# Kernel tuning notes

Measured on AMD Instinct MI355X. Metric: run time of the kernel, lower is better.

## Reference

```python
import math
import jax, jax.numpy as jnp
import numpy as np

EMBED_DIM = 768
NUM_HEADS = 12
HEAD_DIM = EMBED_DIM // NUM_HEADS
NUM_BUCKETS = 32
MAX_DISTANCE = 128
B, S = 8, 1024


def setup_inputs() -> dict:
    key = jax.random.key(0)
    ks = jax.random.split(key, 16)
    sc = 0.02
    d = {
        "query": jax.random.normal(ks[0], (B, S, EMBED_DIM), jnp.float32),
        "Wq": jax.random.normal(ks[1], (EMBED_DIM, EMBED_DIM), jnp.float32) * sc,
        "bq": jnp.zeros((EMBED_DIM,), jnp.float32),
        "Wk": jax.random.normal(ks[2], (EMBED_DIM, EMBED_DIM), jnp.float32) * sc,
        "bk": jnp.zeros((EMBED_DIM,), jnp.float32),
        "Wv": jax.random.normal(ks[3], (EMBED_DIM, EMBED_DIM), jnp.float32) * sc,
        "bv": jnp.zeros((EMBED_DIM,), jnp.float32),
        "Wo": jax.random.normal(ks[4], (EMBED_DIM, EMBED_DIM), jnp.float32) * sc,
        "bo": jnp.zeros((EMBED_DIM,), jnp.float32),
        "rel_embed": jax.random.normal(ks[5], (NUM_BUCKETS, NUM_HEADS), jnp.float32) * sc,
        "gru_W": jax.random.normal(ks[6], (HEAD_DIM, 8), jnp.float32) * sc,
        "gru_b": jnp.zeros((8,), jnp.float32),
        "gru_const": jnp.ones((1, NUM_HEADS, 1, 1), jnp.float32),
    }
    return d


def _rel_pos_bias(rel_embed, seq_len):
    # bidirectional T5-style bucketing, matching WavLM._relative_positions_bucket
    ctx = jnp.arange(seq_len)[:, None]
    mem = jnp.arange(seq_len)[None, :]
    rp = mem - ctx  # [S, S]
    nb = NUM_BUCKETS // 2
    buckets = (rp > 0).astype(jnp.int32) * nb
    arp = jnp.abs(rp)
    max_exact = nb // 2
    is_small = arp < max_exact
    # truncation toward zero == astype for positive values; clamp to avoid log(0)
    large = max_exact + (
        jnp.log(jnp.maximum(arp, 1).astype(jnp.float32) / max_exact)
        / math.log(MAX_DISTANCE / max_exact)
        * (nb - max_exact)
    ).astype(jnp.int32)
    large = jnp.minimum(large, nb - 1)
    buckets = buckets + jnp.where(is_small, arp, large)
    # embedding lookup -> [S, S, H] -> [H, S, S]
    return rel_embed[buckets].transpose(2, 0, 1)


def reference(query, Wq, bq, Wk, bk, Wv, bv, Wo, bo, rel_embed, gru_W, gru_b, gru_const):
    b, s, e = query.shape
    h, d = NUM_HEADS, HEAD_DIM
    pos_bias = _rel_pos_bias(rel_embed, s)  # [H, S, S]

    # GRU-style gate computed from raw query, per head
    ql = query.reshape(b, s, h, d).transpose(0, 2, 1, 3)  # [B, H, S, D]
    g = jax.nn.sigmoid((ql @ gru_W + gru_b).reshape(b, h, s, 2, 4).sum(-1))  # [B,H,S,2]
    gate_a = g[..., 0:1]
    gate_b = g[..., 1:2]
    gate = gate_a * (gate_b * gru_const - 1.0) + 2.0  # [B, H, S, 1]
    attn_mask = gate * pos_bias[None]  # [B, H, S, S]

    scale = d ** (-0.5)
    q = (query @ Wq + bq).reshape(b, s, h, d).transpose(0, 2, 1, 3) * scale
    k = (query @ Wk + bk).reshape(b, s, h, d).transpose(0, 2, 1, 3)
    v = (query @ Wv + bv).reshape(b, s, h, d).transpose(0, 2, 1, 3)

    scores = jnp.einsum("bhqd,bhkd->bhqk", q, k) + attn_mask
    w = jax.nn.softmax(scores, axis=-1)  # max-subtraction in torch is a no-op math-wise
    out = jnp.einsum("bhqk,bhkd->bhqd", w, v)
    out = out.transpose(0, 2, 1, 3).reshape(b, s, h * d)
    return out @ Wo + bo
```

## Files before the change

kernel.cpp:

```cpp
#include <hip/hip_runtime.h>
#include <hip/hip_bf16.h>
#include <math.h>

#define EMBED 768
#define NH 12
#define HD 64
#define SEQ 1024
#define BATCH 8
#define NROWS (BATCH * SEQ)
#define LOG2E 1.44269504088896340736f

typedef __attribute__((ext_vector_type(4))) float f32x4;
typedef __attribute__((ext_vector_type(8))) short short8;
typedef __attribute__((ext_vector_type(8))) _Float16 half8;
typedef unsigned short u16;

__device__ __forceinline__ u16 f2bf(float x) {
    union { float f; unsigned u; } v; v.f = x;
    unsigned r = v.u + 0x7fff + ((v.u >> 16) & 1);
    return (u16)(r >> 16);
}
__device__ __forceinline__ void split2h(float x, u16& hi, u16& lo) {
    _Float16 h = (_Float16)x;
    _Float16 l = (_Float16)(x - (float)h);
    union { _Float16 f; u16 u; } a, b;
    a.f = h; b.f = l;
    hi = a.u; lo = b.u;
}
__device__ __forceinline__ u16 f2h(float x) {
    union { _Float16 f; u16 u; } a; a.f = (_Float16)x; return a.u;
}
__device__ __forceinline__ unsigned pkbf(float a, float b) {
    union { __hip_bfloat162 v; unsigned u; } cv;
    cv.v = __float22bfloat162_rn(make_float2(a, b));
    return cv.u;
}
__device__ __forceinline__ void gll16(const void* g, void* l) {
    __builtin_amdgcn_global_load_lds(
        (const __attribute__((address_space(1))) unsigned int*)g,
        (__attribute__((address_space(3))) unsigned int*)l,
        16, 0, 0);
}

__global__ void bias_table_kernel(const float* __restrict__ rel_embed,
                                  float* __restrict__ bt)
{
    int idx = blockIdx.x * 256 + threadIdx.x;
    const int total = NH * 2047;
    if (idx >= total) return;
    int h    = idx / 2047;
    int dpos = idx - h * 2047;
    int rp   = dpos - 1023;
    int bucket = (rp > 0) ? 16 : 0;
    int arp = rp < 0 ? -rp : rp;
    if (arp < 8) {
        bucket += arp;
    } else {
        double v = log((double)arp / 8.0) / log(16.0) * 8.0;
        int l = 8 + (int)v;
        if (l > 15) l = 15;
        bucket += l;
    }
    bt[idx] = rel_embed[bucket * NH + h] * LOG2E;
}

__global__ void gate_kernel(const float* __restrict__ query,
                            const float* __restrict__ gru_W,
                            const float* __restrict__ gru_b,
                            const float* __restrict__ gru_c,
                            float* __restrict__ gate)
{
    int idx = blockIdx.x * 256 + threadIdx.x;
    if (idx >= BATCH * NH * SEQ) return;
    int s  = idx & (SEQ - 1);
    int bh = idx >> 10;
    int h  = bh % NH;
    int b  = bh / NH;

    const float* x = query + ((size_t)(b * SEQ + s) * EMBED + h * HD);
    float z[8] = {0.f, 0.f, 0.f, 0.f, 0.f, 0.f, 0.f, 0.f};
    for (int d = 0; d < HD; ++d) {
        float xv = x[d];
        const float* wrow = gru_W + d * 8;
        #pragma unroll
        for (int c = 0; c < 8; ++c) z[c] += xv * wrow[c];
    }
    float s0 = (z[0] + gru_b[0]) + (z[1] + gru_b[1]) + (z[2] + gru_b[2]) + (z[3] + gru_b[3]);
    float s1 = (z[4] + gru_b[4]) + (z[5] + gru_b[5]) + (z[6] + gru_b[6]) + (z[7] + gru_b[7]);
    float g0 = 1.f / (1.f + expf(-s0));
    float g1 = 1.f / (1.f + expf(-s1));
    gate[idx] = g0 * (g1 * gru_c[h] - 1.f) + 2.f;
}

__global__ __launch_bounds__(256)
void convertA_h(const float* __restrict__ A, u16* __restrict__ Ah,
                u16* __restrict__ Al)
{
    int idx = (blockIdx.x * 256 + threadIdx.x) * 4;
    float4 v = *(const float4*)(A + idx);
    ushort4 h, l;
    split2h(v.x, h.x, l.x); split2h(v.y, h.y, l.y);
    split2h(v.z, h.z, l.z); split2h(v.w, h.w, l.w);
    *(ushort4*)(Ah + idx) = h;
    *(ushort4*)(Al + idx) = l;
}

__global__ __launch_bounds__(256)
void convertWT_h(const float* __restrict__ W, u16* __restrict__ WT)
{
    __shared__ float tile[32][33];
    int t  = threadIdx.x;
    int k0 = blockIdx.y * 32, n0 = blockIdx.x * 32;
    int r = t >> 3, c = (t & 7) * 4;
    float4 v = *(const float4*)&W[(size_t)(k0 + r) * EMBED + n0 + c];
    tile[r][c] = v.x; tile[r][c + 1] = v.y; tile[r][c + 2] = v.z; tile[r][c + 3] = v.w;
    __syncthreads();
    int n = t >> 3, ks = (t & 7) * 4;
    ushort4 h;
    h.x = f2h(tile[ks    ][n]);
    h.y = f2h(tile[ks + 1][n]);
    h.z = f2h(tile[ks + 2][n]);
    h.w = f2h(tile[ks + 3][n]);
    *(ushort4*)&WT[(size_t)(n0 + n) * EMBED + k0 + ks] = h;
}

__global__ __launch_bounds__(256)
void gemm_h2(const u16* __restrict__ Ah, const u16* __restrict__ Al,
             const u16* __restrict__ BT, const float* __restrict__ bias,
             u16* __restrict__ Cb, float* __restrict__ Cf, float scale)
{
    __shared__ u16 Ah_s[64 * 32];
    __shared__ u16 Al_s[64 * 32];
    __shared__ u16 B_s[128 * 32];

    const int t    = threadIdx.x;
    const int lane = t & 63;
    const int wid  = t >> 6;
    const int L    = lane & 15;
    const int quad = lane >> 4;
    const int row0 = blockIdx.y * 64;
    const int col0 = blockIdx.x * 128;
    const int wm   = (wid >> 1) * 32;
    const int wn   = (wid & 1) * 64;

    f32x4 acc[2][4];
    #pragma unroll
    for (int mt = 0; mt < 2; ++mt)
        #pragma unroll
        for (int nt = 0; nt < 4; ++nt) acc[mt][nt] = (f32x4){0.f, 0.f, 0.f, 0.f};

    const int r_a = t >> 2;
    const int c_a = (t & 3) ^ (r_a & 3);
    const u16* gA_h = Ah + (size_t)(row0 + r_a) * EMBED + 8 * c_a;
    const u16* gA_l = Al + (size_t)(row0 + r_a) * EMBED + 8 * c_a;
    const u16* gB0  = BT + (size_t)(col0 + r_a) * EMBED + 8 * c_a;
    const u16* gB1  = BT + (size_t)(col0 + 64 + r_a) * EMBED + 8 * c_a;
    char* lA_h = (char*)Ah_s + wid * 1024;
    char* lA_l = (char*)Al_s + wid * 1024;
    char* lB   = (char*)B_s  + wid * 1024;

    const int swz = 8 * (quad ^ (L & 3));

    for (int k0 = 0; k0 < EMBED; k0 += 32) {
        __syncthreads();
        gll16(gA_h + k0, lA_h);
        gll16(gA_l + k0, lA_l);
        gll16(gB0  + k0, lB);
        gll16(gB1  + k0, lB + 4096);
        __syncthreads();

        half8 af_h[2], af_l[2], bf[4];
        #pragma unroll
        for (int mt = 0; mt < 2; ++mt) {
            af_h[mt] = *(const half8*)&Ah_s[(wm + mt * 16 + L) * 32 + swz];
            af_l[mt] = *(const half8*)&Al_s[(wm + mt * 16 + L) * 32 + swz];
        }
        #pragma unroll
        for (int nt = 0; nt < 4; ++nt)
            bf[nt] = *(const half8*)&B_s[(wn + nt * 16 + L) * 32 + swz];

        #pragma unroll
        for (int mt = 0; mt < 2; ++mt)
            #pragma unroll
            for (int nt = 0; nt < 4; ++nt) {
                acc[mt][nt] = __builtin_amdgcn_mfma_f32_16x16x32_f16(af_h[mt], bf[nt], acc[mt][nt], 0, 0, 0);
                acc[mt][nt] = __builtin_amdgcn_mfma_f32_16x16x32_f16(af_l[mt], bf[nt], acc[mt][nt], 0, 0, 0);
            }
    }

    float bcol[4];
    #pragma unroll
    for (int nt = 0; nt < 4; ++nt) bcol[nt] = bias[col0 + wn + nt * 16 + L];

    #pragma unroll
    for (int mt = 0; mt < 2; ++mt)
        #pragma unroll
        for (int r = 0; r < 4; ++r) {
            int row = row0 + wm + mt * 16 + quad * 4 + r;
            size_t base = (size_t)row * EMBED + col0 + wn + L;
            if (Cb) {
                #pragma unroll
                for (int nt = 0; nt < 4; ++nt)
                    Cb[base + nt * 16] = f2bf((acc[mt][nt][r] + bcol[nt]) * scale);
            } else {
                #pragma unroll
                for (int nt = 0; nt < 4; ++nt)
                    Cf[base + nt * 16] = (acc[mt][nt][r] + bcol[nt]) * scale;
            }
        }
}

__global__ __launch_bounds__(256)
void attn_mfma2(const u16* __restrict__ Qg, const u16* __restrict__ Kg,
                const u16* __restrict__ Vg, const float* __restrict__ gate,
                const float* __restrict__ bias_tab,
                u16* __restrict__ Oh, u16* __restrict__ Ol)
{
    __shared__ float    bt_lds[2048];
    __shared__ u16      Klds[64 * 64];
    __shared__ unsigned Vt2[64 * 36];
    __shared__ unsigned PB[4][16 * 33];

    const int t    = threadIdx.x;
    const int lane = t & 63;
    const int wid  = t >> 6;
    const int L    = lane & 15;
    const int quad = lane >> 4;

    const int bh = blockIdx.y;
    const int b  = bh / NH;
    const int h  = bh % NH;
    const int qw = blockIdx.x * 128 + wid * 32;

    for (int i = t; i < 2047; i += 256) bt_lds[i] = bias_tab[h * 2047 + i];

    short8 qf[2][2];
    int   qabs[2];
    float g2[2];
    #pragma unroll
    for (int qt = 0; qt < 2; ++qt) {
        qabs[qt] = qw + qt * 16 + L;
        g2[qt]   = gate[(size_t)bh * SEQ + qabs[qt]];
        const u16* qp = Qg + ((size_t)(b * SEQ + qabs[qt]) * EMBED + h * HD + quad * 8);
        qf[qt][0] = *(const short8*)qp;
        qf[qt][1] = *(const short8*)(qp + 32);
    }

    float lac[2] = {0.f, 0.f};
    f32x4 o[4][2];
    #pragma unroll
    for (int dt = 0; dt < 4; ++dt)
        #pragma unroll
        for (int qt = 0; qt < 2; ++qt) o[dt][qt] = (f32x4){0.f, 0.f, 0.f, 0.f};

    const int k_a = t >> 3, c_a = (t & 7) ^ (k_a & 7);
    const int k_b = (t + 256) >> 3, c_b = (t & 7) ^ (k_b & 7);
    const u16* gK0 = Kg + ((size_t)(b * SEQ + k_a) * EMBED + h * HD + 8 * c_a);
    const u16* gK1 = Kg + ((size_t)(b * SEQ + k_b) * EMBED + h * HD + 8 * c_b);
    char* lK0 = (char*)Klds + wid * 1024;
    char* lK1 = (char*)Klds + 4096 + wid * 1024;

    const int vkp = t & 31, vdc = t >> 5;
    const u16* gV = Vg + ((size_t)(b * SEQ + 2 * vkp) * EMBED + h * HD + vdc * 8);

    unsigned* PBw = PB[wid];

    for (int k0 = 0; k0 < SEQ; k0 += 64) {
        __syncthreads();
        gll16(gK0 + (size_t)k0 * EMBED, lK0);
        gll16(gK1 + (size_t)k0 * EMBED, lK1);
        {
            const u16* vp = gV + (size_t)k0 * EMBED;
            union { short8 v; u16 u[8]; } e, odd;
            e.v   = *(const short8*)vp;
            odd.v = *(const short8*)(vp + EMBED);
            #pragma unroll
            for (int j = 0; j < 8; ++j)
                Vt2[(vdc * 8 + j) * 36 + vkp] = (unsigned)e.u[j] | ((unsigned)odd.u[j] << 16);
        }
        __syncthreads();

        f32x4 st[4][2];
        #pragma unroll
        for (int kt = 0; kt < 4; ++kt)
            #pragma unroll
            for (int qt = 0; qt < 2; ++qt) st[kt][qt] = (f32x4){0.f, 0.f, 0.f, 0.f};
        #pragma unroll
        for (int c = 0; c < 2; ++c) {
            #pragma unroll
            for (int kt = 0; kt < 4; ++kt) {
                int krow = kt * 16 + L;
                short8 kf = *(const short8*)&Klds[krow * 64 + 8 * ((c * 4 + quad) ^ (krow & 7))];
                st[kt][0] = __builtin_amdgcn_mfma_f32_16x16x32_bf16(kf, qf[0][c], st[kt][0], 0, 0, 0);
                st[kt][1] = __builtin_amdgcn_mfma_f32_16x16x32_bf16(kf, qf[1][c], st[kt][1], 0, 0, 0);
            }
        }

        #pragma unroll
        for (int c = 0; c < 2; ++c) {
            #pragma unroll
            for (int kt2 = 0; kt2 < 2; ++kt2) {
                int kt = c * 2 + kt2;
                #pragma unroll
                for (int qt = 0; qt < 2; ++qt) {
                    int bidx = k0 + kt * 16 + quad * 4 - qabs[qt] + 1023;
                    float p0 = __builtin_amdgcn_exp2f(st[kt][qt][0] + g2[qt] * bt_lds[bidx + 0]);
                    float p1 = __builtin_amdgcn_exp2f(st[kt][qt][1] + g2[qt] * bt_lds[bidx + 1]);
                    float p2 = __builtin_amdgcn_exp2f(st[kt][qt][2] + g2[qt] * bt_lds[bidx + 2]);
                    float p3 = __builtin_amdgcn_exp2f(st[kt][qt][3] + g2[qt] * bt_lds[bidx + 3]);
                    lac[qt] += (p0 + p1) + (p2 + p3);
                    PBw[(kt2 * 8 + quad * 2 + 0) * 33 + qt * 16 + L] = pkbf(p0, p1);
                    PBw[(kt2 * 8 + quad * 2 + 1) * 33 + qt * 16 + L] = pkbf(p2, p3);
                }
            }
            short8 pb[2];
            #pragma unroll
            for (int qt = 0; qt < 2; ++qt) {
                const unsigned* src = &PBw[(quad * 4) * 33 + qt * 16 + L];
                union { unsigned u[4]; short8 v; } w;
                w.u[0] = src[0];
                w.u[1] = src[33];
                w.u[2] = src[66];
                w.u[3] = src[99];
                pb[qt] = w.v;
            }
            #pragma unroll
            for (int dt = 0; dt < 4; ++dt) {
                short8 vf = *(const short8*)&Vt2[(dt * 16 + L) * 36 + c * 16 + quad * 4];
                o[dt][0] = __builtin_amdgcn_mfma_f32_16x16x32_bf16(vf, pb[0], o[dt][0], 0, 0, 0);
                o[dt][1] = __builtin_amdgcn_mfma_f32_16x16x32_bf16(vf, pb[1], o[dt][1], 0, 0, 0);
            }
        }
    }

    #pragma unroll
    for (int qt = 0; qt < 2; ++qt) {
        lac[qt] += __shfl_xor(lac[qt], 16);
        lac[qt] += __shfl_xor(lac[qt], 32);
    }
    #pragma unroll
    for (int qt = 0; qt < 2; ++qt) {
        float inv = 1.f / lac[qt];
        #pragma unroll
        for (int dt = 0; dt < 4; ++dt) {
            ushort4 h4, l4;
            split2h(o[dt][qt][0] * inv, h4.x, l4.x);
            split2h(o[dt][qt][1] * inv, h4.y, l4.y);
            split2h(o[dt][qt][2] * inv, h4.z, l4.z);
            split2h(o[dt][qt][3] * inv, h4.w, l4.w);
            size_t base = (size_t)(b * SEQ + qabs[qt]) * EMBED + h * HD + dt * 16 + quad * 4;
            *(ushort4*)&Oh[base] = h4;
            *(ushort4*)&Ol[base] = l4;
        }
    }
}

extern "C" void kernel_launch(void* const* d_in, const int* in_sizes, int n_in,
                              void* d_out, int out_size, void* d_ws, size_t ws_size,
                              hipStream_t stream)
{
    (void)in_sizes; (void)n_in; (void)out_size; (void)ws_size;
    const float* query = (const float*)d_in[0];
    const float* Wq    = (const float*)d_in[1];
    const float* bq    = (const float*)d_in[2];
    const float* Wk    = (const float*)d_in[3];
    const float* bk    = (const float*)d_in[4];
    const float* Wv    = (const float*)d_in[5];
    const float* bv    = (const float*)d_in[6];
    const float* Wo    = (const float*)d_in[7];
    const float* bo    = (const float*)d_in[8];
    const float* rel   = (const float*)d_in[9];
    const float* gruW  = (const float*)d_in[10];
    const float* gruB  = (const float*)d_in[11];
    const float* gruC  = (const float*)d_in[12];
    float* out = (float*)d_out;

    const size_t NE = (size_t)NROWS * EMBED;
    const size_t WN = (size_t)EMBED * EMBED;
    u16* ws   = (u16*)d_ws;
    u16* Ah   = ws;
    u16* Al   = Ah + NE;
    u16* WqT  = Al + NE;
    u16* WkT  = WqT + WN;
    u16* WvT  = WkT + WN;
    u16* WoT  = WvT + WN;
    u16* Qb   = WoT + WN;
    u16* Kb   = Qb + NE;
    u16* Vb   = Kb + NE;
    u16* Ohb  = Vb + NE;
    u16* Olb  = Ohb + NE;
    float* gate = (float*)(Olb + NE);
    float* bt   = gate + (size_t)BATCH * NH * SEQ;

    bias_table_kernel<<<(NH * 2047 + 255) / 256, 256, 0, stream>>>(rel, bt);
    gate_kernel<<<(BATCH * NH * SEQ + 255) / 256, 256, 0, stream>>>(query, gruW, gruB, gruC, gate);

    convertA_h<<<NE / 1024, 256, 0, stream>>>(query, Ah, Al);
    dim3 wt(EMBED / 32, EMBED / 32);
    convertWT_h<<<wt, 256, 0, stream>>>(Wq, WqT);
    convertWT_h<<<wt, 256, 0, stream>>>(Wk, WkT);
    convertWT_h<<<wt, 256, 0, stream>>>(Wv, WvT);
    convertWT_h<<<wt, 256, 0, stream>>>(Wo, WoT);

    dim3 gg(EMBED / 128, NROWS / 64);
    gemm_h2<<<gg, 256, 0, stream>>>(Ah, Al, WqT, bq, Qb, nullptr, 0.125f * LOG2E);
    gemm_h2<<<gg, 256, 0, stream>>>(Ah, Al, WkT, bk, Kb, nullptr, 1.0f);
    gemm_h2<<<gg, 256, 0, stream>>>(Ah, Al, WvT, bv, Vb, nullptr, 1.0f);

    attn_mfma2<<<dim3(SEQ / 128, BATCH * NH), 256, 0, stream>>>(Qb, Kb, Vb, gate, bt, Ohb, Olb);

    gemm_h2<<<gg, 256, 0, stream>>>(Ohb, Olb, WoT, bo, nullptr, out, 1.0f);
}
```

Baseline: 302.0 us.

## Fuse QKV projections, emit transposed V, and streamline attention LDS layouts

Merges the three Q/K/V projection GEMMs into one kernel that loads each A tile once and multiplies it against all three weight tiles. The V output is written transposed per head so the attention kernel can copy it straight into LDS with async loads instead of repacking it in registers. The P buffer is reorganised for vectorised stores and loads, and the bias table is stored as float2 pairs to halve LDS reads. Row tiles shrink to 32 (more blocks) and the transposed V writes are scattered 8-byte stores, which could hurt coalescing.

```diff
diff --git a/kernel.cpp b/kernel.cpp
--- a/kernel.cpp
+++ b/kernel.cpp
@@ -125,114 +125,204 @@
 }
 
 __global__ __launch_bounds__(256)
-void gemm_h2(const u16* __restrict__ Ah, const u16* __restrict__ Al,
-             const u16* __restrict__ BT, const float* __restrict__ bias,
-             u16* __restrict__ Cb, float* __restrict__ Cf, float scale)
-{
-    __shared__ u16 Ah_s[64 * 32];
-    __shared__ u16 Al_s[64 * 32];
-    __shared__ u16 B_s[128 * 32];
+void gemm_qkv(const u16* __restrict__ Ah, const u16* __restrict__ Al,
+              const u16* __restrict__ WqT, const u16* __restrict__ WkT,
+              const u16* __restrict__ WvT,
+              const float* __restrict__ bq, const float* __restrict__ bk,
+              const float* __restrict__ bv,
+              u16* __restrict__ Qb, u16* __restrict__ Kb, u16* __restrict__ VT,
+              float qscale)
+{
+    __shared__ u16 Ah_s[32 * 32];
+    __shared__ u16 Al_s[32 * 32];
+    __shared__ u16 Bq_s[128 * 32];
+    __shared__ u16 Bk_s[128 * 32];
+    __shared__ u16 Bv_s[128 * 32];
 
     const int t    = threadIdx.x;
     const int lane = t & 63;
     const int wid  = t >> 6;
     const int L    = lane & 15;
     const int quad = lane >> 4;
-    const int row0 = blockIdx.y * 64;
+    const int row0 = blockIdx.y * 32;
     const int col0 = blockIdx.x * 128;
-    const int wm   = (wid >> 1) * 32;
+    const int wm   = (wid >> 1) * 16;
     const int wn   = (wid & 1) * 64;
 
-    f32x4 acc[2][4];
-    #pragma unroll
-    for (int mt = 0; mt < 2; ++mt)
-        #pragma unroll
-        for (int nt = 0; nt < 4; ++nt) acc[mt][nt] = (f32x4){0.f, 0.f, 0.f, 0.f};
-
-    const int r_a = t >> 2;
-    const int c_a = (t & 3) ^ (r_a & 3);
-    const u16* gA_h = Ah + (size_t)(row0 + r_a) * EMBED + 8 * c_a;
-    const u16* gA_l = Al + (size_t)(row0 + r_a) * EMBED + 8 * c_a;
-    const u16* gB0  = BT + (size_t)(col0 + r_a) * EMBED + 8 * c_a;
-    const u16* gB1  = BT + (size_t)(col0 + 64 + r_a) * EMBED + 8 * c_a;
-    char* lA_h = (char*)Ah_s + wid * 1024;
-    char* lA_l = (char*)Al_s + wid * 1024;
-    char* lB   = (char*)B_s  + wid * 1024;
+    f32x4 accQ[4], accK[4], accV[4];
+    #pragma unroll
+    for (int nt = 0; nt < 4; ++nt) {
+        accQ[nt] = (f32x4){0.f, 0.f, 0.f, 0.f};
+        accK[nt] = (f32x4){0.f, 0.f, 0.f, 0.f};
+        accV[nt] = (f32x4){0.f, 0.f, 0.f, 0.f};
+    }
+
+    const int rA = (wid & 1) * 16 + (lane >> 2);
+    const int cA = (lane & 3) ^ (rA & 3);
+    const u16* gA = ((wid < 2) ? Ah : Al) + (size_t)(row0 + rA) * EMBED + 8 * cA;
+    char* lA = (char*)((wid < 2) ? Ah_s : Al_s) + (wid & 1) * 1024;
+
+    const int rB = t >> 2;
+    const int cB = (t & 3) ^ (rB & 3);
+    const size_t bo0 = (size_t)(col0 + rB) * EMBED + 8 * cB;
+    const size_t bo1 = (size_t)(col0 + 64 + rB) * EMBED + 8 * cB;
+    char* lBq = (char*)Bq_s + wid * 1024;
+    char* lBk = (char*)Bk_s + wid * 1024;
+    char* lBv = (char*)Bv_s + wid * 1024;
 
     const int swz = 8 * (quad ^ (L & 3));
 
     for (int k0 = 0; k0 < EMBED; k0 += 32) {
         __syncthreads();
-        gll16(gA_h + k0, lA_h);
-        gll16(gA_l + k0, lA_l);
-        gll16(gB0  + k0, lB);
-        gll16(gB1  + k0, lB + 4096);
-        __syncthreads();
-
-        half8 af_h[2], af_l[2], bf[4];
-        #pragma unroll
-        for (int mt = 0; mt < 2; ++mt) {
-            af_h[mt] = *(const half8*)&Ah_s[(wm + mt * 16 + L) * 32 + swz];
-            af_l[mt] = *(const half8*)&Al_s[(wm + mt * 16 + L) * 32 + swz];
-        }
-        #pragma unroll
-        for (int nt = 0; nt < 4; ++nt)
-            bf[nt] = *(const half8*)&B_s[(wn + nt * 16 + L) * 32 + swz];
-
-        #pragma unroll
-        for (int mt = 0; mt < 2; ++mt)
-            #pragma unroll
-            for (int nt = 0; nt < 4; ++nt) {
-                acc[mt][nt] = __builtin_amdgcn_mfma_f32_16x16x32_f16(af_h[mt], bf[nt], acc[mt][nt], 0, 0, 0);
-                acc[mt][nt] = __builtin_amdgcn_mfma_f32_16x16x32_f16(af_l[mt], bf[nt], acc[mt][nt], 0, 0, 0);
-            }
-    }
-
-    float bcol[4];
-    #pragma unroll
-    for (int nt = 0; nt < 4; ++nt) bcol[nt] = bias[col0 + wn + nt * 16 + L];
-
-    #pragma unroll
-    for (int mt = 0; mt < 2; ++mt)
-        #pragma unroll
-        for (int r = 0; r < 4; ++r) {
-            int row = row0 + wm + mt * 16 + quad * 4 + r;
-            size_t base = (size_t)row * EMBED + col0 + wn + L;
-            if (Cb) {
-                #pragma unroll
-                for (int nt = 0; nt < 4; ++nt)
-                    Cb[base + nt * 16] = f2bf((acc[mt][nt][r] + bcol[nt]) * scale);
-            } else {
-                #pragma unroll
-                for (int nt = 0; nt < 4; ++nt)
-                    Cf[base + nt * 16] = (acc[mt][nt][r] + bcol[nt]) * scale;
-            }
-        }
+        gll16(gA + k0, lA);
+        gll16(WqT + bo0 + k0, lBq); gll16(WqT + bo1 + k0, lBq + 4096);
+        gll16(WkT + bo0 + k0, lBk); gll16(WkT + bo1 + k0, lBk + 4096);
+        gll16(WvT + bo0 + k0, lBv); gll16(WvT + bo1 + k0, lBv + 4096);
+        __syncthreads();
+
+        half8 ah = *(const half8*)&Ah_s[(wm + L) * 32 + swz];
+        half8 al = *(const half8*)&Al_s[(wm + L) * 32 + swz];
+        #pragma unroll
+        for (int nt = 0; nt < 4; ++nt) {
+            const int boff = (wn + nt * 16 + L) * 32 + swz;
+            half8 b0 = *(const half8*)&Bq_s[boff];
+            accQ[nt] = __builtin_amdgcn_mfma_f32_16x16x32_f16(ah, b0, accQ[nt], 0, 0, 0);
+            accQ[nt] = __builtin_amdgcn_mfma_f32_16x16x32_f16(al, b0, accQ[nt], 0, 0, 0);
+            half8 b1 = *(const half8*)&Bk_s[boff];
+            accK[nt] = __builtin_amdgcn_mfma_f32_16x16x32_f16(ah, b1, accK[nt], 0, 0, 0);
+            accK[nt] = __builtin_amdgcn_mfma_f32_16x16x32_f16(al, b1, accK[nt], 0, 0, 0);
+            half8 b2 = *(const half8*)&Bv_s[boff];
+            accV[nt] = __builtin_amdgcn_mfma_f32_16x16x32_f16(ah, b2, accV[nt], 0, 0, 0);
+            accV[nt] = __builtin_amdgcn_mfma_f32_16x16x32_f16(al, b2, accV[nt], 0, 0, 0);
+        }
+    }
+
+    float bq4[4], bk4[4], bv4[4];
+    #pragma unroll
+    for (int nt = 0; nt < 4; ++nt) {
+        int n = col0 + wn + nt * 16 + L;
+        bq4[nt] = bq[n]; bk4[nt] = bk[n]; bv4[nt] = bv[n];
+    }
+
+    const int rowa = row0 + wm + quad * 4;
+    #pragma unroll
+    for (int r = 0; r < 4; ++r) {
+        size_t base = (size_t)(rowa + r) * EMBED + col0 + wn + L;
+        #pragma unroll
+        for (int nt = 0; nt < 4; ++nt) {
+            Qb[base + nt * 16] = f2bf((accQ[nt][r] + bq4[nt]) * qscale);
+            Kb[base + nt * 16] = f2bf(accK[nt][r] + bk4[nt]);
+        }
+    }
+    {
+        int b_  = rowa >> 10;
+        int s0_ = rowa & 1023;
+        #pragma unroll
+        for (int nt = 0; nt < 4; ++nt) {
+            int n = col0 + wn + nt * 16 + L;
+            int hh = n >> 6, dd = n & 63;
+            ushort4 pk;
+            pk.x = f2bf(accV[nt][0] + bv4[nt]);
+            pk.y = f2bf(accV[nt][1] + bv4[nt]);
+            pk.z = f2bf(accV[nt][2] + bv4[nt]);
+            pk.w = f2bf(accV[nt][3] + bv4[nt]);
+            *(ushort4*)&VT[((size_t)(b_ * NH + hh) * HD + dd) * SEQ + s0_] = pk;
+        }
+    }
 }
 
 __global__ __launch_bounds__(256)
-void attn_mfma2(const u16* __restrict__ Qg, const u16* __restrict__ Kg,
-                const u16* __restrict__ Vg, const float* __restrict__ gate,
-                const float* __restrict__ bias_tab,
-                u16* __restrict__ Oh, u16* __restrict__ Ol)
-{
-    __shared__ float    bt_lds[2048];
-    __shared__ u16      Klds[64 * 64];
-    __shared__ unsigned Vt2[64 * 36];
-    __shared__ unsigned PB[4][16 * 33];
+void gemm_out(const u16* __restrict__ Ah, const u16* __restrict__ Al,
+              const u16* __restrict__ BT, const float* __restrict__ bias,
+              float* __restrict__ C)
+{
+    __shared__ u16 Ah_s[32 * 32];
+    __shared__ u16 Al_s[32 * 32];
+    __shared__ u16 B_s[128 * 32];
 
     const int t    = threadIdx.x;
     const int lane = t & 63;
     const int wid  = t >> 6;
     const int L    = lane & 15;
     const int quad = lane >> 4;
+    const int row0 = blockIdx.y * 32;
+    const int col0 = blockIdx.x * 128;
+    const int wm   = (wid >> 1) * 16;
+    const int wn   = (wid & 1) * 64;
+
+    f32x4 acc[4];
+    #pragma unroll
+    for (int nt = 0; nt < 4; ++nt) acc[nt] = (f32x4){0.f, 0.f, 0.f, 0.f};
+
+    const int rA = (wid & 1) * 16 + (lane >> 2);
+    const int cA = (lane & 3) ^ (rA & 3);
+    const u16* gA = ((wid < 2) ? Ah : Al) + (size_t)(row0 + rA) * EMBED + 8 * cA;
+    char* lA = (char*)((wid < 2) ? Ah_s : Al_s) + (wid & 1) * 1024;
+
+    const int rB = t >> 2;
+    const int cB = (t & 3) ^ (rB & 3);
+    const u16* gB0 = BT + (size_t)(col0 + rB) * EMBED + 8 * cB;
+    const u16* gB1 = BT + (size_t)(col0 + 64 + rB) * EMBED + 8 * cB;
+    char* lB = (char*)B_s + wid * 1024;
+
+    const int swz = 8 * (quad ^ (L & 3));
+
+    for (int k0 = 0; k0 < EMBED; k0 += 32) {
+        __syncthreads();
+        gll16(gA  + k0, lA);
+        gll16(gB0 + k0, lB);
+        gll16(gB1 + k0, lB + 4096);
+        __syncthreads();
+
+        half8 ah = *(const half8*)&Ah_s[(wm + L) * 32 + swz];
+        half8 al = *(const half8*)&Al_s[(wm + L) * 32 + swz];
+        #pragma unroll
+        for (int nt = 0; nt < 4; ++nt) {
+            half8 b = *(const half8*)&B_s[(wn + nt * 16 + L) * 32 + swz];
+            acc[nt] = __builtin_amdgcn_mfma_f32_16x16x32_f16(ah, b, acc[nt], 0, 0, 0);
+            acc[nt] = __builtin_amdgcn_mfma_f32_16x16x32_f16(al, b, acc[nt], 0, 0, 0);
+        }
+    }
+
+    float b4[4];
+    #pragma unroll
+    for (int nt = 0; nt < 4; ++nt) b4[nt] = bias[col0 + wn + nt * 16 + L];
+    #pragma unroll
+    for (int r = 0; r < 4; ++r) {
+        size_t base = (size_t)(row0 + wm + quad * 4 + r) * EMBED + col0 + wn + L;
+        #pragma unroll
+        for (int nt = 0; nt < 4; ++nt)
+            C[base + nt * 16] = acc[nt][r] + b4[nt];
+    }
+}
+
+__global__ __launch_bounds__(256)
+void attn_mfma3(const u16* __restrict__ Qg, const u16* __restrict__ Kg,
+                const u16* __restrict__ VTg, const float* __restrict__ gate,
+                const float* __restrict__ bias_tab,
+                u16* __restrict__ Oh, u16* __restrict__ Ol)
+{
+    __shared__ float2   btP[2047];
+    __shared__ u16      Klds[64 * 64];
+    __shared__ u16      Vlds[64 * 64];
+    __shared__ unsigned PB[4][32 * 20];
+
+    const int t    = threadIdx.x;
+    const int lane = t & 63;
+    const int wid  = t >> 6;
+    const int L    = lane & 15;
+    const int quad = lane >> 4;
 
     const int bh = blockIdx.y;
     const int b  = bh / NH;
     const int h  = bh % NH;
     const int qw = blockIdx.x * 128 + wid * 32;
 
-    for (int i = t; i < 2047; i += 256) bt_lds[i] = bias_tab[h * 2047 + i];
+    for (int i = t; i < 2047; i += 256) {
+        float a  = bias_tab[h * 2047 + i];
+        float nb = (i < 2046) ? bias_tab[h * 2047 + i + 1] : 0.f;
+        btP[i] = make_float2(a, nb);
+    }
 
     short8 qf[2][2];
     int   qabs[2];
@@ -254,14 +344,16 @@
         for (int qt = 0; qt < 2; ++qt) o[dt][qt] = (f32x4){0.f, 0.f, 0.f, 0.f};
 
     const int k_a = t >> 3, c_a = (t & 7) ^ (k_a & 7);
-    const int k_b = (t + 256) >> 3, c_b = (t & 7) ^ (k_b & 7);
     const u16* gK0 = Kg + ((size_t)(b * SEQ + k_a) * EMBED + h * HD + 8 * c_a);
-    const u16* gK1 = Kg + ((size_t)(b * SEQ + k_b) * EMBED + h * HD + 8 * c_b);
+    const u16* gK1 = Kg + ((size_t)(b * SEQ + 32 + k_a) * EMBED + h * HD + 8 * c_a);
     char* lK0 = (char*)Klds + wid * 1024;
     char* lK1 = (char*)Klds + 4096 + wid * 1024;
 
-    const int vkp = t & 31, vdc = t >> 5;
-    const u16* gV = Vg + ((size_t)(b * SEQ + 2 * vkp) * EMBED + h * HD + vdc * 8);
+    const int d_a = t >> 3, cv_a = (t & 7) ^ (d_a & 7);
+    const u16* gV0 = VTg + ((size_t)(bh * HD + d_a) * SEQ + 8 * cv_a);
+    const u16* gV1 = VTg + ((size_t)(bh * HD + 32 + d_a) * SEQ + 8 * cv_a);
+    char* lV0 = (char*)Vlds + wid * 1024;
+    char* lV1 = (char*)Vlds + 4096 + wid * 1024;
 
     unsigned* PBw = PB[wid];
 
@@ -269,15 +361,8 @@
         __syncthreads();
         gll16(gK0 + (size_t)k0 * EMBED, lK0);
         gll16(gK1 + (size_t)k0 * EMBED, lK1);
-        {
-            const u16* vp = gV + (size_t)k0 * EMBED;
-            union { short8 v; u16 u[8]; } e, odd;
-            e.v   = *(const short8*)vp;
-            odd.v = *(const short8*)(vp + EMBED);
-            #pragma unroll
-            for (int j = 0; j < 8; ++j)
-                Vt2[(vdc * 8 + j) * 36 + vkp] = (unsigned)e.u[j] | ((unsigned)odd.u[j] << 16);
-        }
+        gll16(gV0 + k0, lV0);
+        gll16(gV1 + k0, lV1);
         __syncthreads();
 
         f32x4 st[4][2];
@@ -304,29 +389,30 @@
                 #pragma unroll
                 for (int qt = 0; qt < 2; ++qt) {
                     int bidx = k0 + kt * 16 + quad * 4 - qabs[qt] + 1023;
-                    float p0 = __builtin_amdgcn_exp2f(st[kt][qt][0] + g2[qt] * bt_lds[bidx + 0]);
-                    float p1 = __builtin_amdgcn_exp2f(st[kt][qt][1] + g2[qt] * bt_lds[bidx + 1]);
-                    float p2 = __builtin_amdgcn_exp2f(st[kt][qt][2] + g2[qt] * bt_lds[bidx + 2]);
-                    float p3 = __builtin_amdgcn_exp2f(st[kt][qt][3] + g2[qt] * bt_lds[bidx + 3]);
+                    float2 u = btP[bidx];
+                    float2 v = btP[bidx + 2];
+                    float p0 = __builtin_amdgcn_exp2f(st[kt][qt][0] + g2[qt] * u.x);
+                    float p1 = __builtin_amdgcn_exp2f(st[kt][qt][1] + g2[qt] * u.y);
+                    float p2 = __builtin_amdgcn_exp2f(st[kt][qt][2] + g2[qt] * v.x);
+                    float p3 = __builtin_amdgcn_exp2f(st[kt][qt][3] + g2[qt] * v.y);
                     lac[qt] += (p0 + p1) + (p2 + p3);
-                    PBw[(kt2 * 8 + quad * 2 + 0) * 33 + qt * 16 + L] = pkbf(p0, p1);
-                    PBw[(kt2 * 8 + quad * 2 + 1) * 33 + qt * 16 + L] = pkbf(p2, p3);
+                    uint2 w;
+                    w.x = pkbf(p0, p1);
+                    w.y = pkbf(p2, p3);
+                    *(uint2*)&PBw[(qt * 16 + L) * 20 + kt2 * 8 + quad * 2] = w;
                 }
             }
             short8 pb[2];
             #pragma unroll
             for (int qt = 0; qt < 2; ++qt) {
-                const unsigned* src = &PBw[(quad * 4) * 33 + qt * 16 + L];
-                union { unsigned u[4]; short8 v; } w;
-                w.u[0] = src[0];
-                w.u[1] = src[33];
-                w.u[2] = src[66];
-                w.u[3] = src[99];
+                union { uint4 u4; short8 v; } w;
+                w.u4 = *(const uint4*)&PBw[(qt * 16 + L) * 20 + quad * 4];
                 pb[qt] = w.v;
             }
             #pragma unroll
             for (int dt = 0; dt < 4; ++dt) {
-                short8 vf = *(const short8*)&Vt2[(dt * 16 + L) * 36 + c * 16 + quad * 4];
+                int drow = dt * 16 + L;
+                short8 vf = *(const short8*)&Vlds[drow * 64 + 8 * ((c * 4 + quad) ^ (drow & 7))];
                 o[dt][0] = __builtin_amdgcn_mfma_f32_16x16x32_bf16(vf, pb[0], o[dt][0], 0, 0, 0);
                 o[dt][1] = __builtin_amdgcn_mfma_f32_16x16x32_bf16(vf, pb[1], o[dt][1], 0, 0, 0);
             }
@@ -386,8 +472,8 @@
     u16* WoT  = WvT + WN;
     u16* Qb   = WoT + WN;
     u16* Kb   = Qb + NE;
-    u16* Vb   = Kb + NE;
-    u16* Ohb  = Vb + NE;
+    u16* VT   = Kb + NE;
+    u16* Ohb  = VT + NE;
     u16* Olb  = Ohb + NE;
     float* gate = (float*)(Olb + NE);
     float* bt   = gate + (size_t)BATCH * NH * SEQ;
@@ -402,12 +488,11 @@
     convertWT_h<<<wt, 256, 0, stream>>>(Wv, WvT);
     convertWT_h<<<wt, 256, 0, stream>>>(Wo, WoT);
 
-    dim3 gg(EMBED / 128, NROWS / 64);
-    gemm_h2<<<gg, 256, 0, stream>>>(Ah, Al, WqT, bq, Qb, nullptr, 0.125f * LOG2E);
-    gemm_h2<<<gg, 256, 0, stream>>>(Ah, Al, WkT, bk, Kb, nullptr, 1.0f);
-    gemm_h2<<<gg, 256, 0, stream>>>(Ah, Al, WvT, bv, Vb, nullptr, 1.0f);
-
-    attn_mfma2<<<dim3(SEQ / 128, BATCH * NH), 256, 0, stream>>>(Qb, Kb, Vb, gate, bt, Ohb, Olb);
-
-    gemm_h2<<<gg, 256, 0, stream>>>(Ohb, Olb, WoT, bo, nullptr, out, 1.0f);
-}
+    dim3 gq(EMBED / 128, NROWS / 32);
+    gemm_qkv<<<gq, 256, 0, stream>>>(Ah, Al, WqT, WkT, WvT, bq, bk, bv,
+                                     Qb, Kb, VT, 0.125f * LOG2E);
+
+    attn_mfma3<<<dim3(SEQ / 128, BATCH * NH), 256, 0, stream>>>(Qb, Kb, VT, gate, bt, Ohb, Olb);
+
+    gemm_out<<<gq, 256, 0, stream>>>(Ohb, Olb, WoT, bo, out);
+}
```

Result: no change. 298.1 us (-1.3%).
